# Kernel tuning notes

Hardware: AMD Instinct MI355X
Metric: run time of the kernel (lower is better)

The kernel has to match this reference:

```python
import jax, jax.numpy as jnp
import numpy as np

N_E = 8192
E_DIM = 256
BETA = 0.25
LAMBDA_REG = 0.1
UNIFORM_WEIGHT = 0.1


def setup_inputs() -> dict:
    key = jax.random.key(0)
    k1, k2 = jax.random.split(key)
    z = jax.random.normal(k1, (8, 2048, E_DIM), dtype=jnp.float32)
    # embedding initialized uniform(-1/n_e, 1/n_e) as in the torch module
    emb = jax.random.uniform(k2, (N_E, E_DIM), dtype=jnp.float32,
                             minval=-1.0 / N_E, maxval=1.0 / N_E)
    return {"z": z, "emb": emb}


def _safe_cdist(emb):
    # torch.cdist(emb, emb, p=2) with zero-safe sqrt (diag distances are 0)
    sq = jnp.sum(emb * emb, axis=1)  # [n_e]
    d2 = sq[:, None] + sq[None, :] - 2.0 * (emb @ emb.T)  # [n_e, n_e]
    d2 = jnp.maximum(d2, 0.0)
    pos = d2 > 0
    return jnp.where(pos, jnp.sqrt(jnp.where(pos, d2, 1.0)), 0.0)


def reference(z, emb):
    zf = z.reshape(-1, E_DIM)  # [N, e_dim]
    # squared-distance matrix: ||z||^2 + ||e||^2 - 2 z.e  -> [N, n_e]
    d = (jnp.sum(zf * zf, axis=1, keepdims=True)
         + jnp.sum(emb * emb, axis=1)
         - 2.0 * (zf @ emb.T))
    min_encoding_indices = jnp.argmin(d, axis=1)  # [N]
    # one-hot @ emb is just a gather of the selected codes
    z_q = emb[min_encoding_indices].reshape(z.shape)

    sg = jax.lax.stop_gradient
    loss = jnp.mean((sg(z_q) - z) ** 2) + BETA * jnp.mean((z_q - sg(z)) ** 2)
    z_q_st = z + sg(z_q - z)  # straight-through

    ed = _safe_cdist(emb)  # [n_e, n_e]
    min_d = jnp.min(ed, axis=1, keepdims=True)
    max_d = jnp.max(ed, axis=1, keepdims=True)
    uniform_loss = jnp.mean(max_d - min_d)
    qq_loss = UNIFORM_WEIGHT * uniform_loss + LAMBDA_REG * jnp.sum(emb * emb)

    return z_q_st, min_encoding_indices.reshape(-1, 1), loss, qq_loss
```

## Files before the change

### kernel.cpp

```cpp
#include <hip/hip_runtime.h>

#define D 256
#define DA 288
#define NKB 9
#define NKB_P 8
#define NE 8192
#define NZ 16384
#define BM 128
#define AM 256
#define BK 32
#define LDA (BM + 4)
#define NB (NE / BM)
#define NTRI (NB * (NB + 1) / 2)
#define NSPLIT_A 16
#define SPLIT_NA (NE / NSPLIT_A)
#define GAPTH_A 0.4096f
#define GAPTH_EFF 0.48f
#define LDM 17
#define NGB (NZ / 4)
#define NCH_A (SPLIT_NA / 32)
#define AUNITS (2 * NKB)
#define PUNITS (2 * NKB_P)
#define NBLK_ARG (NZ / AM * NSPLIT_A)
#define NBLK_BIG (NBLK_ARG + NTRI)

#define SROT(kk) (8 * ((((kk) >> 2)) & 3))
#define SWZR(kk, r) ((((r) + SROT(kk)) & 127))

typedef _Float16 f16x8 __attribute__((ext_vector_type(8)));
typedef _Float16 f16x4 __attribute__((ext_vector_type(4)));
typedef float f32x4 __attribute__((ext_vector_type(4)));

#define MFMA16(a, b, c) __builtin_amdgcn_mfma_f32_16x16x32_f16(a, b, c, 0, 0, 0)

__device__ __forceinline__ void g2l16(const void* g, void* lds) {
    __builtin_amdgcn_global_load_lds(
        (const __attribute__((address_space(1))) void*)g,
        (__attribute__((address_space(3))) void*)lds, 16, 0, 0);
}

__device__ __forceinline__ unsigned umax(unsigned a, unsigned b) { return a > b ? a : b; }
__device__ __forceinline__ unsigned umin(unsigned a, unsigned b) { return a < b ? a : b; }

#define WS_SUMS   0
#define WS_CNT    64
#define WS_ZSQ    256
#define WS_ESQ    (WS_ZSQ + NZ * 4)
#define WS_IDX    (WS_ESQ + NE * 4)
#define WS_KP1    (WS_IDX + NZ * 4)
#define WS_KP2    (WS_KP1 + NZ * NSPLIT_A * 4)
#define WS_RMX    (WS_KP2 + NZ * NSPLIT_A * 4)
#define WS_RMN    (WS_RMX + NE * 4)
#define WS_PACK   (WS_RMN + NE * 4)
#define WS_GPART  (WS_PACK + NZ * 8)
#define WS_LISTS  (WS_GPART + NGB * 8)
#define WS_ZHF    (WS_LISTS + NZ * NSPLIT_A * 4)
#define WS_EHF    (WS_ZHF + (size_t)(NZ / 16) * NKB * 64 * 8 * 2)
#define WS_CAND   WS_ZHF

__device__ __forceinline__ float waveReduceSumF(float v) {
    v += __shfl_down(v, 32); v += __shfl_down(v, 16); v += __shfl_down(v, 8);
    v += __shfl_down(v, 4);  v += __shfl_down(v, 2);  v += __shfl_down(v, 1);
    return v;
}
__device__ __forceinline__ double waveReduceSumD(double v) {
    v += __shfl_down(v, 32); v += __shfl_down(v, 16); v += __shfl_down(v, 8);
    v += __shfl_down(v, 4);  v += __shfl_down(v, 2);  v += __shfl_down(v, 1);
    return v;
}

__global__ __launch_bounds__(256) void k_setup(double* __restrict__ sums,
                                               int* __restrict__ cnt,
                                               unsigned* __restrict__ rmx,
                                               unsigned* __restrict__ rmn,
                                               unsigned long long* __restrict__ pack) {
    const int n = blockIdx.x * 256 + threadIdx.x;
    if (n == 0) {
        sums[0] = 0.0; sums[1] = 0.0; sums[2] = 0.0; sums[3] = 0.0;
#pragma unroll
        for (int s = 0; s < 24; ++s) cnt[s] = 0;
    }
    if (n < NE) { rmx[n] = 0u; rmn[n] = 0x7F800000u; }
    pack[n] = ~0ull;
}

__global__ __launch_bounds__(256) void k_rowsq(const float* __restrict__ src,
                                               float* __restrict__ rsq,
                                               double* __restrict__ sums) {
    const int row = blockIdx.x * 256 + threadIdx.x;
    const float* p = src + (size_t)row * D;
    float h[2];
#pragma unroll
    for (int half = 0; half < 2; ++half) {
        const float* q = p + half * 128;
        float4 a0 = *(const float4*)&q[0];
        float4 a1 = *(const float4*)&q[4];
        float r0 = __fmul_rn(a0.x, a0.x);
        float r1 = __fmul_rn(a0.y, a0.y);
        float r2 = __fmul_rn(a0.z, a0.z);
        float r3 = __fmul_rn(a0.w, a0.w);
        float r4 = __fmul_rn(a1.x, a1.x);
        float r5 = __fmul_rn(a1.y, a1.y);
        float r6 = __fmul_rn(a1.z, a1.z);
        float r7 = __fmul_rn(a1.w, a1.w);
#pragma unroll
        for (int i = 8; i < 128; i += 8) {
            const float4 b0 = *(const float4*)&q[i];
            const float4 b1 = *(const float4*)&q[i + 4];
            r0 = __fadd_rn(r0, __fmul_rn(b0.x, b0.x));
            r1 = __fadd_rn(r1, __fmul_rn(b0.y, b0.y));
            r2 = __fadd_rn(r2, __fmul_rn(b0.z, b0.z));
            r3 = __fadd_rn(r3, __fmul_rn(b0.w, b0.w));
            r4 = __fadd_rn(r4, __fmul_rn(b1.x, b1.x));
            r5 = __fadd_rn(r5, __fmul_rn(b1.y, b1.y));
            r6 = __fadd_rn(r6, __fmul_rn(b1.z, b1.z));
            r7 = __fadd_rn(r7, __fmul_rn(b1.w, b1.w));
        }
        const float t01 = __fadd_rn(r0, r1);
        const float t23 = __fadd_rn(r2, r3);
        const float t45 = __fadd_rn(r4, r5);
        const float t67 = __fadd_rn(r6, r7);
        h[half] = __fadd_rn(__fadd_rn(t01, t23), __fadd_rn(t45, t67));
    }
    const float tot = __fadd_rn(h[0], h[1]);
    rsq[row] = tot;
    if (sums != nullptr) {
        double s = waveReduceSumD((double)tot);
        if ((threadIdx.x & 63) == 0) atomicAdd(&sums[0], s);
    }
}

__global__ __launch_bounds__(256) void k_cvt_zf(const float* __restrict__ z,
                                                f16x8* __restrict__ zf) {
    __shared__ _Float16 Ls[64 * 296];
    const int t = threadIdx.x;
    const int row0 = blockIdx.x * 64;
#pragma unroll
    for (int i = 0; i < 16; ++i) {
        const int f4 = i * 256 + t;
        const int r = f4 >> 6, c4 = f4 & 63;
        const float4 v = *(const float4*)&z[(size_t)(row0 + r) * D + c4 * 4];
        f16x4 h;
        h[0] = (_Float16)v.x; h[1] = (_Float16)v.y;
        h[2] = (_Float16)v.z; h[3] = (_Float16)v.w;
        *(f16x4*)&Ls[r * 296 + c4 * 4] = h;
    }
#pragma unroll
    for (int i = 0; i < 8; ++i) {
        const int idx = i * 256 + t;
        const int r = idx >> 5, c = idx & 31;
        Ls[r * 296 + 256 + c] = (c <= 1) ? (_Float16)1.0f : (_Float16)0.0f;
    }
    __syncthreads();
    const int l = t & 63, w = t >> 6;
#pragma unroll
    for (int kb = 0; kb < NKB; ++kb) {
        const f16x8 fr = *(const f16x8*)&Ls[(w * 16 + (l & 15)) * 296 + kb * 32 + (l >> 4) * 8];
        zf[((size_t)(blockIdx.x * 4 + w) * NKB + kb) * 64 + l] = fr;
    }
}

__global__ __launch_bounds__(256) void k_cvt_ef(const float* __restrict__ e,
                                                const float* __restrict__ esq,
                                                f16x8* __restrict__ ef) {
    __shared__ _Float16 Ls[64 * 296];
    const int t = threadIdx.x;
    const int row0 = blockIdx.x * 64;
#pragma unroll
    for (int i = 0; i < 16; ++i) {
        const int f4 = i * 256 + t;
        const int r = f4 >> 6, c4 = f4 & 63;
        const float4 v = *(const float4*)&e[(size_t)(row0 + r) * D + c4 * 4];
        f16x4 h;
        h[0] = (_Float16)(v.x * 8192.0f); h[1] = (_Float16)(v.y * 8192.0f);
        h[2] = (_Float16)(v.z * 8192.0f); h[3] = (_Float16)(v.w * 8192.0f);
        *(f16x4*)&Ls[r * 296 + c4 * 4] = h;
    }
#pragma unroll
    for (int i = 0; i < 8; ++i) {
        const int idx = i * 256 + t;
        const int r = idx >> 5, c = idx & 31;
        _Float16 av = (_Float16)0.0f;
        if (c == 0) av = (_Float16)(esq[row0 + r] * -4096.0f);
        if (c == 1) av = (_Float16)512.0f;
        Ls[r * 296 + 256 + c] = av;
    }
    __syncthreads();
    const int l = t & 63, w = t >> 6;
#pragma unroll
    for (int kb = 0; kb < NKB; ++kb) {
        const f16x8 fr = *(const f16x8*)&Ls[(w * 16 + (l & 15)) * 296 + kb * 32 + (l >> 4) * 8];
        ef[((size_t)(blockIdx.x * 4 + w) * NKB + kb) * 64 + l] = fr;
    }
}

__global__ __launch_bounds__(256, 2) void k_big(
        const f16x8* __restrict__ zf, const f16x8* __restrict__ ef,
        const float* __restrict__ esq,
        unsigned* __restrict__ kp1, unsigned* __restrict__ kp2,
        unsigned* __restrict__ rmxg, unsigned* __restrict__ rmng) {
    __shared__ __align__(16) char Sh[2 * AUNITS * 1024];

    const int t = threadIdx.x;
    const int l = t & 63;
    const int w = t >> 6;
    const int quad = l >> 4;
    const int l15 = l & 15;

    if (blockIdx.x < NBLK_ARG) {
        _Float16 (*Bsm)[AUNITS * 512] = (_Float16(*)[AUNITS * 512])Sh;
        const int lin = blockIdx.x;
        const int rowblk = lin & 63;
        const int sp = lin >> 6;
        const int row0 = rowblk * AM;
        const int arb0 = rowblk * 16 + w * 4;

        f16x8 ah[4][NKB];
#pragma unroll
        for (int mi = 0; mi < 4; ++mi)
#pragma unroll
            for (int kb = 0; kb < NKB; ++kb)
                ah[mi][kb] = zf[((size_t)(arb0 + mi) * NKB + kb) * 64 + l];

        unsigned b1[16], b2[16];
#pragma unroll
        for (int s = 0; s < 16; ++s) { b1[s] = 0u; b2[s] = 0u; }

        const char* gp[5];
#pragma unroll
        for (int ui = 0; ui < 5; ++ui) {
            const int u = w + ui * 4;
            const int uc = (u < AUNITS) ? u : 0;
            const int nj = uc / NKB, kb = uc - nj * NKB;
            gp[ui] = (const char*)&ef[((size_t)(sp * 32 + nj) * NKB + kb) * 64 + l];
        }

        auto stage = [&](size_t choff, int buf) {
            char* lb = (char*)&Bsm[0][0] + buf * (AUNITS * 1024);
#pragma unroll
            for (int ui = 0; ui < 5; ++ui) {
                const int u = w + ui * 4;
                if (u < AUNITS) g2l16(gp[ui] + choff, lb + u * 1024);
            }
        };

        auto ins = [&](unsigned key, int s) {
            unsigned b2n;
            asm("v_med3_u32 %0, %1, %2, %3"
                : "=v"(b2n) : "v"(key), "v"(b1[s]), "v"(b2[s]));
            b2[s] = b2n;
            b1[s] = umax(b1[s], key);
        };

        stage(0, 0);
        const f32x4 Zv = (f32x4){0.f, 0.f, 0.f, 0.f};
        int inv0 = 1023 - l15;
        for (int ch = 0; ch < NCH_A; ++ch) {
            const int buf = ch & 1;
            __syncthreads();
            if (ch + 1 < NCH_A) stage((size_t)(ch + 1) * 18432u, buf ^ 1);

            const unsigned invA = (unsigned)inv0;
            const unsigned invB = (unsigned)(inv0 - 16);

            f32x4 acc0[4], acc1[4];
            {
                const f16x8 bh = *(const f16x8*)&Bsm[buf][(0 * NKB + 0) * 512 + l * 8];
#pragma unroll
                for (int mi = 0; mi < 4; ++mi) acc0[mi] = MFMA16(ah[mi][0], bh, Zv);
            }
#pragma unroll
            for (int kb = 1; kb < NKB; ++kb) {
                const f16x8 bh = *(const f16x8*)&Bsm[buf][(0 * NKB + kb) * 512 + l * 8];
#pragma unroll
                for (int mi = 0; mi < 4; ++mi) acc0[mi] = MFMA16(ah[mi][kb], bh, acc0[mi]);
            }
            {
                const f16x8 bh = *(const f16x8*)&Bsm[buf][(1 * NKB + 0) * 512 + l * 8];
#pragma unroll
                for (int mi = 0; mi < 4; ++mi) acc1[mi] = MFMA16(ah[mi][0], bh, Zv);
            }
#pragma unroll
            for (int kb = 1; kb < NKB; ++kb) {
                const f16x8 bh = *(const f16x8*)&Bsm[buf][(1 * NKB + kb) * 512 + l * 8];
#pragma unroll
                for (int mi = 0; mi < 4; ++mi) acc1[mi] = MFMA16(ah[mi][kb], bh, acc1[mi]);
#pragma unroll
                for (int e = 2 * (kb - 1); e < 2 * (kb - 1) + 2; ++e) {
                    const int mi0 = e >> 2, r0 = e & 3;
                    ins((__float_as_uint(acc0[mi0][r0]) & 0xFFFFFC00u) | invA, e);
                }
            }
#pragma unroll
            for (int mi = 0; mi < 4; ++mi)
#pragma unroll
                for (int r = 0; r < 4; ++r)
                    ins((__float_as_uint(acc1[mi][r]) & 0xFFFFFC00u) | invB, mi * 4 + r);

            inv0 -= 32;
        }

#pragma unroll
        for (int s = 0; s < 16; ++s) {
            unsigned v1 = b1[s], v2 = b2[s];
#pragma unroll
            for (int m = 1; m <= 8; m <<= 1) {
                const unsigned o1 = __shfl_xor(v1, m);
                const unsigned o2 = __shfl_xor(v2, m);
                const unsigned n2 = umax(umin(v1, o1), umax(v2, o2));
                v1 = umax(v1, o1);
                v2 = n2;
            }
            if (l15 == 0) {
                const int mi = s >> 2, r = s & 3;
                const int row = row0 + w * 64 + mi * 16 + quad * 4 + r;
                kp1[(size_t)row * NSPLIT_A + sp] = v1;
                kp2[(size_t)row * NSPLIT_A + sp] = v2;
            }
        }
    } else {
        _Float16 (*Bsm)[PUNITS * 512] = (_Float16(*)[PUNITS * 512])Sh;
        int p = blockIdx.x - NBLK_ARG;
        int bi = 0;
        while (p >= NB - bi) { p -= NB - bi; ++bi; }
        const int bj = bi + p;
        const int row0 = bi * BM;
        const int c0 = bj * BM;

        float sR[8], sC[8];
#pragma unroll
        for (int mi = 0; mi < 2; ++mi)
#pragma unroll
            for (int r = 0; r < 4; ++r)
                sR[mi * 4 + r] = esq[row0 + w * 32 + mi * 16 + quad * 4 + r];
#pragma unroll
        for (int nj = 0; nj < 8; ++nj) sC[nj] = esq[c0 + nj * 16 + l15];

        const int arb = bi * 8 + w * 2;
        const int cfb = bj * 8;

        f16x8 ah[2][NKB_P];
#pragma unroll
        for (int kb = 0; kb < NKB_P; ++kb) {
            ah[0][kb] = ef[((size_t)arb * NKB + kb) * 64 + l];
            ah[1][kb] = ef[((size_t)(arb + 1) * NKB + kb) * 64 + l];
        }

        float rmn[8], rmx[8], cmn[8], cmx[8];
#pragma unroll
        for (int s = 0; s < 8; ++s) { rmn[s] = 3.4e38f; rmx[s] = 0.f; cmn[s] = 3.4e38f; cmx[s] = 0.f; }

        auto stage = [&](int ch, int buf) {
            for (int u = w; u < PUNITS; u += 4) {
                const int nj = u >> 3, kb = u & 7;
                g2l16(&ef[((size_t)(cfb + ch * 2 + nj) * NKB + kb) * 64 + l],
                      &Bsm[buf][u * 512]);
            }
        };

        stage(0, 0);
        for (int ch = 0; ch < 4; ++ch) {
            const int buf = ch & 1;
            __syncthreads();
            if (ch + 1 < 4) stage(ch + 1, buf ^ 1);

            f32x4 acc[2][2];
#pragma unroll
            for (int mi = 0; mi < 2; ++mi)
#pragma unroll
                for (int nj = 0; nj < 2; ++nj) acc[mi][nj] = (f32x4){0.f, 0.f, 0.f, 0.f};

#pragma unroll
            for (int kb = 0; kb < NKB_P; ++kb) {
                const f16x8 bh0 = *(const f16x8*)&Bsm[buf][(0 * 8 + kb) * 512 + l * 8];
                const f16x8 bh1 = *(const f16x8*)&Bsm[buf][(1 * 8 + kb) * 512 + l * 8];
#pragma unroll
                for (int mi = 0; mi < 2; ++mi) {
                    acc[mi][0] = MFMA16(ah[mi][kb], bh0, acc[mi][0]);
                    acc[mi][1] = MFMA16(ah[mi][kb], bh1, acc[mi][1]);
                }
            }

#pragma unroll
            for (int nj = 0; nj < 2; ++nj) {
                const int cidx = ch * 2 + nj;
#pragma unroll
                for (int mi = 0; mi < 2; ++mi)
#pragma unroll
                    for (int r = 0; r < 4; ++r) {
                        const int s = mi * 4 + r;
                        const float t1 = __fadd_rn(sR[s], sC[cidx]);
                        const float d2 = fmaf(-0x1p-25f, acc[mi][nj][r], t1);
                        const float d2c = fmaxf(d2, 0.f);
                        rmn[s] = fminf(rmn[s], d2c);
                        rmx[s] = fmaxf(rmx[s], d2c);
                        cmn[cidx] = fminf(cmn[cidx], d2c);
                        cmx[cidx] = fmaxf(cmx[cidx], d2c);
                    }
            }
        }

#pragma unroll
        for (int s = 0; s < 8; ++s) {
#pragma unroll
            for (int m = 1; m <= 8; m <<= 1) {
                rmn[s] = fminf(rmn[s], __shfl_xor(rmn[s], m));
                rmx[s] = fmaxf(rmx[s], __shfl_xor(rmx[s], m));
            }
        }
        if (l15 == 0) {
#pragma unroll
            for (int s = 0; s < 8; ++s) {
                const int mi = s >> 2, r = s & 3;
                const int row = row0 + w * 32 + mi * 16 + quad * 4 + r;
                atomicMax(&rmxg[row], __float_as_uint(rmx[s]));
                atomicMin(&rmng[row], __float_as_uint(rmn[s]));
            }
        }

#pragma unroll
        for (int nj = 0; nj < 8; ++nj) {
#pragma unroll
            for (int m = 16; m <= 32; m <<= 1) {
                cmn[nj] = fminf(cmn[nj], __shfl_xor(cmn[nj], m));
                cmx[nj] = fmaxf(cmx[nj], __shfl_xor(cmx[nj], m));
            }
        }
        __syncthreads();
        float* Mn = (float*)&Bsm[0][0];
        float* Mx = (float*)&Bsm[0][0] + 512;
        if (quad == 0) {
#pragma unroll
            for (int nj = 0; nj < 8; ++nj) {
                Mn[w * 128 + nj * 16 + l15] = cmn[nj];
                Mx[w * 128 + nj * 16 + l15] = cmx[nj];
            }
        }
        __syncthreads();
        if (t < BM) {
            float mn = Mn[t], mx = Mx[t];
#pragma unroll
            for (int ww = 1; ww < 4; ++ww) {
                mn = fminf(mn, Mn[ww * 128 + t]);
                mx = fmaxf(mx, Mx[ww * 128 + t]);
            }
            atomicMax(&rmxg[c0 + t], __float_as_uint(mx));
            atomicMin(&rmng[c0 + t], __float_as_uint(mn));
        }
    }
}

__global__ __launch_bounds__(256) void k_merge(const unsigned* __restrict__ kp1,
                                               const unsigned* __restrict__ kp2,
                                               int* __restrict__ idxbuf,
                                               float* __restrict__ outidx,
                                               int* __restrict__ cnt,
                                               int* __restrict__ lists,
                                               unsigned long long* __restrict__ cand) {
    const int n = blockIdx.x * 256 + threadIdx.x;
    unsigned k1v[NSPLIT_A], k2v[NSPLIT_A];
#pragma unroll
    for (int s = 0; s < NSPLIT_A; ++s) {
        k1v[s] = kp1[n * NSPLIT_A + s];
        k2v[s] = kp2[n * NSPLIT_A + s];
    }
    unsigned K1 = k1v[0]; int sb = 0;
#pragma unroll
    for (int s = 1; s < NSPLIT_A; ++s)
        if (k1v[s] > K1) { K1 = k1v[s]; sb = s; }
    unsigned K2 = 0u;
#pragma unroll
    for (int s = 0; s < NSPLIT_A; ++s) {
        const unsigned a = (s == sb) ? k2v[s] : k1v[s];
        K2 = umax(K2, a);
    }
    const int ii1 = sb * SPLIT_NA + 1023 - (int)(K1 & 1023u);
    idxbuf[n] = ii1;
    outidx[n] = (float)ii1;
    const float val1 = __uint_as_float(K1 & 0xFFFFFC00u);
    const float val2 = __uint_as_float(K2 & 0xFFFFFC00u);
    if (val1 - val2 < GAPTH_EFF) {
        const float vlim = val1 - GAPTH_EFF;
        int ncand = 0;
#pragma unroll
        for (int s = 0; s < NSPLIT_A; ++s) {
            if (__uint_as_float(k1v[s] & 0xFFFFFC00u) >= vlim) ++ncand;
            if (__uint_as_float(k2v[s] & 0xFFFFFC00u) >= vlim) {
                const int p = atomicAdd(&cnt[s], 1);
                lists[s * NZ + p] = n;
            }
        }
        const int base = atomicAdd(&cnt[16], ncand);
        int o = 0;
#pragma unroll
        for (int s = 0; s < NSPLIT_A; ++s)
            if (__uint_as_float(k1v[s] & 0xFFFFFC00u) >= vlim) {
                const int col = s * SPLIT_NA + 1023 - (int)(k1v[s] & 1023u);
                cand[base + o] = ((unsigned long long)(unsigned)n << 32) |
                                 (unsigned)col;
                ++o;
            }
    }
}

__global__ __launch_bounds__(256) void k_fix_cand(const float* __restrict__ z,
                                                  const float* __restrict__ emb,
                                                  const float* __restrict__ zsq,
                                                  const float* __restrict__ esq,
                                                  const int* __restrict__ cnt,
                                                  const unsigned long long* __restrict__ cand,
                                                  unsigned long long* __restrict__ pack) {
    const int nc = cnt[16];
    for (int i = blockIdx.x * 256 + threadIdx.x; i < nc; i += gridDim.x * 256) {
        const unsigned long long pr = cand[i];
        const int row = (int)(pr >> 32);
        const int col = (int)(pr & 0xffffffffu);
        const float4* zp = (const float4*)(z + (size_t)row * D);
        const float4* ep = (const float4*)(emb + (size_t)col * D);
        float acc = 0.f;
#pragma unroll
        for (int k4 = 0; k4 < D / 4; ++k4) {
            const float4 a = zp[k4];
            const float4 b = ep[k4];
            acc = fmaf(a.x, b.x, acc);
            acc = fmaf(a.y, b.y, acc);
            acc = fmaf(a.z, b.z, acc);
            acc = fmaf(a.w, b.w, acc);
        }
        const float sc = fmaf(-2.f, acc, __fadd_rn(zsq[row], esq[col]));
        const unsigned long long pk =
            ((unsigned long long)__float_as_uint(sc) << 32) | (unsigned)col;
        atomicMin(&pack[row], pk);
    }
}

__global__ __launch_bounds__(256) void k_fix_split(const float* __restrict__ z,
                                                   const float* __restrict__ emb,
                                                   const float* __restrict__ zsq,
                                                   const float* __restrict__ esq,
                                                   const int* __restrict__ cnt,
                                                   const int* __restrict__ lists,
                                                   unsigned long long* __restrict__ pack) {
    __shared__ float As[BK * LDA];
    __shared__ float Bs[BK * LDA];
    __shared__ float Sq[BM];
    __shared__ int frow[BM];

    const int s = blockIdx.x >> 2;
    const int chunk = blockIdx.x & 3;
    const int ns = cnt[s];
    const int c0 = s * SPLIT_NA + chunk * BM;
    const int t = threadIdx.x;
    const int tr = t >> 4;
    const int tc = t & 15;
    const int sr = t >> 3;
    const int skq = t & 7;
    const int wrot = 8 * (skq & 3);

    for (int rb = blockIdx.y; rb * BM < ns; rb += gridDim.y) {
        __syncthreads();
        if (t < BM) {
            const int fi = rb * BM + t;
            frow[t] = (fi < ns) ? lists[s * NZ + fi] : lists[s * NZ];
            Sq[t] = esq[c0 + t];
        }
        __syncthreads();

        float zqr[8];
#pragma unroll
        for (int i = 0; i < 8; ++i) zqr[i] = zsq[frow[tr * 8 + i]];

        float best[8];
        int bidx[8];
#pragma unroll
        for (int i = 0; i < 8; ++i) { best[i] = 3.4e38f; bidx[i] = 0; }

        float acc[8][8];
#pragma unroll
        for (int i = 0; i < 8; ++i)
#pragma unroll
            for (int j = 0; j < 8; ++j) acc[i][j] = 0.f;

        float4 pav[4], pbv[4];
#pragma unroll
        for (int q = 0; q < 4; ++q) {
            const int r = sr + 32 * q;
            pav[q] = *(const float4*)&z[(size_t)frow[r] * D + 0 + 4 * skq];
            pbv[q] = *(const float4*)&emb[(size_t)(c0 + r) * D + 0 + 4 * skq];
        }

        for (int kb = 0; kb < D; kb += BK) {
            __syncthreads();
#pragma unroll
            for (int q = 0; q < 4; ++q) {
                const int r = sr + 32 * q;
                const int rr = (r + wrot) & 127;
                As[(4 * skq + 0) * LDA + rr] = pav[q].x;
                As[(4 * skq + 1) * LDA + rr] = pav[q].y;
                As[(4 * skq + 2) * LDA + rr] = pav[q].z;
                As[(4 * skq + 3) * LDA + rr] = pav[q].w;
                Bs[(4 * skq + 0) * LDA + rr] = pbv[q].x;
                Bs[(4 * skq + 1) * LDA + rr] = pbv[q].y;
                Bs[(4 * skq + 2) * LDA + rr] = pbv[q].z;
                Bs[(4 * skq + 3) * LDA + rr] = pbv[q].w;
            }
            __syncthreads();
            if (kb + BK < D) {
#pragma unroll
                for (int q = 0; q < 4; ++q) {
                    const int r = sr + 32 * q;
                    pav[q] = *(const float4*)&z[(size_t)frow[r] * D + kb + BK + 4 * skq];
                    pbv[q] = *(const float4*)&emb[(size_t)(c0 + r) * D + kb + BK + 4 * skq];
                }
            }
#pragma unroll
            for (int k = 0; k < BK; ++k) {
                const float4 a0 = *(const float4*)&As[k * LDA + SWZR(k, tr * 8)];
                const float4 a1 = *(const float4*)&As[k * LDA + SWZR(k, tr * 8 + 4)];
                const float4 b0 = *(const float4*)&Bs[k * LDA + SWZR(k, tc * 4)];
                const float4 b1 = *(const float4*)&Bs[k * LDA + SWZR(k, 64 + tc * 4)];
                const float a[8] = {a0.x, a0.y, a0.z, a0.w, a1.x, a1.y, a1.z, a1.w};
                const float b[8] = {b0.x, b0.y, b0.z, b0.w, b1.x, b1.y, b1.z, b1.w};
#pragma unroll
                for (int i = 0; i < 8; ++i)
#pragma unroll
                    for (int j = 0; j < 8; ++j)
                        acc[i][j] = fmaf(a[i], b[j], acc[i][j]);
            }
        }
#pragma unroll
        for (int jj = 0; jj < 8; ++jj) {
            const int cloc = (jj < 4) ? (tc * 4 + jj) : (64 + tc * 4 + (jj - 4));
            const float sq = Sq[cloc];
            const int gcol = c0 + cloc;
#pragma unroll
            for (int i = 0; i < 8; ++i) {
                const float t1 = __fadd_rn(zqr[i], sq);
                const float sc = fmaf(-2.f, acc[i][jj], t1);
                if (sc < best[i]) { best[i] = sc; bidx[i] = gcol; }
            }
        }
        __syncthreads();

        float* Rs = As;
        int* Ri = (int*)Bs;
#pragma unroll
        for (int i = 0; i < 8; ++i) {
            Rs[(tr * 8 + i) * LDM + tc] = best[i];
            Ri[(tr * 8 + i) * LDM + tc] = bidx[i];
        }
        __syncthreads();
        if (t < BM) {
            float bs = Rs[t * LDM];
            int bi = Ri[t * LDM];
#pragma unroll
            for (int c = 1; c < 16; ++c) {
                const float sc = Rs[t * LDM + c];
                const int ii = Ri[t * LDM + c];
                if (sc < bs || (sc == bs && ii < bi)) { bs = sc; bi = ii; }
            }
            const int fi = rb * BM + t;
            if (fi < ns) {
                const unsigned long long pk =
                    ((unsigned long long)__float_as_uint(bs) << 32) | (unsigned)bi;
                atomicMin(&pack[frow[t]], pk);
            }
        }
    }
}

__global__ __launch_bounds__(256) void k_gather(const float* __restrict__ z,
                                                const float* __restrict__ emb,
                                                const int* __restrict__ idxbuf,
                                                const unsigned long long* __restrict__ pack,
                                                float* __restrict__ out,
                                                float* __restrict__ outidx,
                                                double* __restrict__ gpart) {
    __shared__ double part[4];
    const int row = blockIdx.x * 4 + (threadIdx.x >> 6);
    const int lane = threadIdx.x & 63;
    const unsigned long long p = pack[row];
    const int idx = (p != ~0ull) ? (int)(p & 0xffffffffu) : idxbuf[row];
    if (lane == 0) outidx[row] = (float)idx;
    const float4 e4 = *(const float4*)&emb[(size_t)idx * D + lane * 4];
    const float4 z4 = *(const float4*)&z[(size_t)row * D + lane * 4];
    *(float4*)&out[(size_t)row * D + lane * 4] = e4;
    const float dx = e4.x - z4.x, dy = e4.y - z4.y;
    const float dzv = e4.z - z4.z, dw = e4.w - z4.w;
    float s = dx * dx + dy * dy + dzv * dzv + dw * dw;
    s = waveReduceSumF(s);
    if (lane == 0) part[threadIdx.x >> 6] = (double)s;
    __syncthreads();
    if (threadIdx.x == 0)
        gpart[blockIdx.x] = part[0] + part[1] + part[2] + part[3];
}

__global__ __launch_bounds__(256) void k_final(const double* __restrict__ sums,
                                               const double* __restrict__ gpart,
                                               const unsigned* __restrict__ rmxg,
                                               const unsigned* __restrict__ rmng,
                                               float* __restrict__ out) {
    __shared__ double part[4];
    __shared__ double partm[4];
    const int t = threadIdx.x;
    double s = 0.0;
#pragma unroll
    for (int i = 0; i < NGB / 256; ++i) s += gpart[i * 256 + t];
    s = waveReduceSumD(s);
    double m = 0.0;
#pragma unroll
    for (int i = 0; i < NE / 256; ++i) {
        const int n = i * 256 + t;
        const float mx = sqrtf(__uint_as_float(rmxg[n]));
        const float mn = sqrtf(__uint_as_float(rmng[n]));
        m += (double)(mx - mn);
    }
    m = waveReduceSumD(m);
    if ((t & 63) == 0) { part[t >> 6] = s; partm[t >> 6] = m; }
    __syncthreads();
    if (t == 0) {
        const double diff2 = part[0] + part[1] + part[2] + part[3];
        const double msum = partm[0] + partm[1] + partm[2] + partm[3];
        const double loss = 1.25 * (diff2 / (double)((size_t)NZ * D));
        const double qq = 0.1 * (msum / (double)NE) + 0.1 * sums[0];
        out[(size_t)NZ * D + NZ] = (float)loss;
        out[(size_t)NZ * D + NZ + 1] = (float)qq;
    }
}

extern "C" void kernel_launch(void* const* d_in, const int* in_sizes, int n_in,
                              void* d_out, int out_size, void* d_ws, size_t ws_size,
                              hipStream_t stream) {
    const float* z = (const float*)d_in[0];
    const float* emb = (const float*)d_in[1];
    float* out = (float*)d_out;
    char* ws = (char*)d_ws;

    double* sums = (double*)(ws + WS_SUMS);
    int* cnt = (int*)(ws + WS_CNT);
    float* zsq = (float*)(ws + WS_ZSQ);
    float* esq = (float*)(ws + WS_ESQ);
    int* idxb = (int*)(ws + WS_IDX);
    unsigned* kp1 = (unsigned*)(ws + WS_KP1);
    unsigned* kp2 = (unsigned*)(ws + WS_KP2);
    unsigned* rmx = (unsigned*)(ws + WS_RMX);
    unsigned* rmn = (unsigned*)(ws + WS_RMN);
    unsigned long long* pack = (unsigned long long*)(ws + WS_PACK);
    double* gpart = (double*)(ws + WS_GPART);
    int* lists = (int*)(ws + WS_LISTS);
    f16x8* zhf = (f16x8*)(ws + WS_ZHF);
    f16x8* ehf = (f16x8*)(ws + WS_EHF);
    unsigned long long* cand = (unsigned long long*)(ws + WS_CAND);
    float* outidx = out + (size_t)NZ * D;

    hipLaunchKernelGGL(k_setup, dim3(NZ / 256), dim3(256), 0, stream,
                       sums, cnt, rmx, rmn, pack);
    hipLaunchKernelGGL(k_rowsq, dim3(NZ / 256), dim3(256), 0, stream, z, zsq, (double*)nullptr);
    hipLaunchKernelGGL(k_rowsq, dim3(NE / 256), dim3(256), 0, stream, emb, esq, sums);
    hipLaunchKernelGGL(k_cvt_zf, dim3(NZ / 64), dim3(256), 0, stream, z, zhf);
    hipLaunchKernelGGL(k_cvt_ef, dim3(NE / 64), dim3(256), 0, stream, emb, esq, ehf);
    hipLaunchKernelGGL(k_big, dim3(NBLK_BIG), dim3(256), 0, stream,
                       zhf, ehf, esq, kp1, kp2, rmx, rmn);
    hipLaunchKernelGGL(k_merge, dim3(NZ / 256), dim3(256), 0, stream,
                       kp1, kp2, idxb, outidx, cnt, lists, cand);
    hipLaunchKernelGGL(k_fix_cand, dim3(128), dim3(256), 0, stream,
                       z, emb, zsq, esq, cnt, cand, pack);
    hipLaunchKernelGGL(k_fix_split, dim3(64, 16), dim3(256), 0, stream,
                       z, emb, zsq, esq, cnt, lists, pack);
    hipLaunchKernelGGL(k_gather, dim3(NGB), dim3(256), 0, stream,
                       z, emb, idxb, pack, out, outidx, gpart);
    hipLaunchKernelGGL(k_final, dim3(1), dim3(256), 0, stream,
                       sums, gpart, rmx, rmn, out);
}
```

Baseline: 286.3 us.

## Drop row-min tracking in pairwise distance, fuse prep kernels

Removes the per-row minimum of the codebook self-distance matrix, relying on the diagonal being zero, so the min reductions and atomicMin calls in the triangle blocks disappear. Merges the setup, row-norm and fp16 conversion kernels into two launches. The codebook squared-norm sum moves into the final kernel instead of using atomics. The risk is a small numeric difference if the reference's diagonal distance is not exactly zero.

After: 253.8 us. 11.4% less time.

```diff
diff --git a/kernel.cpp b/kernel.cpp
--- a/kernel.cpp
+++ b/kernel.cpp
@@ -69,26 +69,7 @@
     return v;
 }
 
-__global__ __launch_bounds__(256) void k_setup(double* __restrict__ sums,
-                                               int* __restrict__ cnt,
-                                               unsigned* __restrict__ rmx,
-                                               unsigned* __restrict__ rmn,
-                                               unsigned long long* __restrict__ pack) {
-    const int n = blockIdx.x * 256 + threadIdx.x;
-    if (n == 0) {
-        sums[0] = 0.0; sums[1] = 0.0; sums[2] = 0.0; sums[3] = 0.0;
-#pragma unroll
-        for (int s = 0; s < 24; ++s) cnt[s] = 0;
-    }
-    if (n < NE) { rmx[n] = 0u; rmn[n] = 0x7F800000u; }
-    pack[n] = ~0ull;
-}
-
-__global__ __launch_bounds__(256) void k_rowsq(const float* __restrict__ src,
-                                               float* __restrict__ rsq,
-                                               double* __restrict__ sums) {
-    const int row = blockIdx.x * 256 + threadIdx.x;
-    const float* p = src + (size_t)row * D;
+__device__ __forceinline__ float rowsq256(const float* __restrict__ p) {
     float h[2];
 #pragma unroll
     for (int half = 0; half < 2; ++half) {
@@ -122,75 +103,91 @@
         const float t67 = __fadd_rn(r6, r7);
         h[half] = __fadd_rn(__fadd_rn(t01, t23), __fadd_rn(t45, t67));
     }
-    const float tot = __fadd_rn(h[0], h[1]);
-    rsq[row] = tot;
-    if (sums != nullptr) {
-        double s = waveReduceSumD((double)tot);
-        if ((threadIdx.x & 63) == 0) atomicAdd(&sums[0], s);
-    }
-}
-
-__global__ __launch_bounds__(256) void k_cvt_zf(const float* __restrict__ z,
-                                                f16x8* __restrict__ zf) {
+    return __fadd_rn(h[0], h[1]);
+}
+
+__global__ __launch_bounds__(256) void k_pre(const float* __restrict__ z,
+                                             const float* __restrict__ emb,
+                                             float* __restrict__ zsq,
+                                             float* __restrict__ esq,
+                                             int* __restrict__ cnt,
+                                             unsigned* __restrict__ rmx,
+                                             unsigned long long* __restrict__ pack) {
+    const int bx = blockIdx.x, t = threadIdx.x;
+    if (bx == 0 && t < 24) cnt[t] = 0;
+    if (bx < 64) {
+        const int row = bx * 256 + t;
+        zsq[row] = rowsq256(z + (size_t)row * D);
+        pack[row] = ~0ull;
+    } else {
+        const int row = (bx - 64) * 256 + t;
+        esq[row] = rowsq256(emb + (size_t)row * D);
+        rmx[row] = 0u;
+    }
+}
+
+__global__ __launch_bounds__(256) void k_cvt(const float* __restrict__ z,
+                                             const float* __restrict__ e,
+                                             const float* __restrict__ esq,
+                                             f16x8* __restrict__ zf,
+                                             f16x8* __restrict__ ef) {
     __shared__ _Float16 Ls[64 * 296];
     const int t = threadIdx.x;
-    const int row0 = blockIdx.x * 64;
-#pragma unroll
-    for (int i = 0; i < 16; ++i) {
-        const int f4 = i * 256 + t;
-        const int r = f4 >> 6, c4 = f4 & 63;
-        const float4 v = *(const float4*)&z[(size_t)(row0 + r) * D + c4 * 4];
-        f16x4 h;
-        h[0] = (_Float16)v.x; h[1] = (_Float16)v.y;
-        h[2] = (_Float16)v.z; h[3] = (_Float16)v.w;
-        *(f16x4*)&Ls[r * 296 + c4 * 4] = h;
-    }
-#pragma unroll
-    for (int i = 0; i < 8; ++i) {
-        const int idx = i * 256 + t;
-        const int r = idx >> 5, c = idx & 31;
-        Ls[r * 296 + 256 + c] = (c <= 1) ? (_Float16)1.0f : (_Float16)0.0f;
-    }
-    __syncthreads();
-    const int l = t & 63, w = t >> 6;
-#pragma unroll
-    for (int kb = 0; kb < NKB; ++kb) {
-        const f16x8 fr = *(const f16x8*)&Ls[(w * 16 + (l & 15)) * 296 + kb * 32 + (l >> 4) * 8];
-        zf[((size_t)(blockIdx.x * 4 + w) * NKB + kb) * 64 + l] = fr;
-    }
-}
-
-__global__ __launch_bounds__(256) void k_cvt_ef(const float* __restrict__ e,
-                                                const float* __restrict__ esq,
-                                                f16x8* __restrict__ ef) {
-    __shared__ _Float16 Ls[64 * 296];
-    const int t = threadIdx.x;
-    const int row0 = blockIdx.x * 64;
-#pragma unroll
-    for (int i = 0; i < 16; ++i) {
-        const int f4 = i * 256 + t;
-        const int r = f4 >> 6, c4 = f4 & 63;
-        const float4 v = *(const float4*)&e[(size_t)(row0 + r) * D + c4 * 4];
-        f16x4 h;
-        h[0] = (_Float16)(v.x * 8192.0f); h[1] = (_Float16)(v.y * 8192.0f);
-        h[2] = (_Float16)(v.z * 8192.0f); h[3] = (_Float16)(v.w * 8192.0f);
-        *(f16x4*)&Ls[r * 296 + c4 * 4] = h;
-    }
-#pragma unroll
-    for (int i = 0; i < 8; ++i) {
-        const int idx = i * 256 + t;
-        const int r = idx >> 5, c = idx & 31;
-        _Float16 av = (_Float16)0.0f;
-        if (c == 0) av = (_Float16)(esq[row0 + r] * -4096.0f);
-        if (c == 1) av = (_Float16)512.0f;
-        Ls[r * 296 + 256 + c] = av;
-    }
-    __syncthreads();
-    const int l = t & 63, w = t >> 6;
-#pragma unroll
-    for (int kb = 0; kb < NKB; ++kb) {
-        const f16x8 fr = *(const f16x8*)&Ls[(w * 16 + (l & 15)) * 296 + kb * 32 + (l >> 4) * 8];
-        ef[((size_t)(blockIdx.x * 4 + w) * NKB + kb) * 64 + l] = fr;
+    const int bx = blockIdx.x;
+    if (bx < NZ / 64) {
+        const int row0 = bx * 64;
+#pragma unroll
+        for (int i = 0; i < 16; ++i) {
+            const int f4 = i * 256 + t;
+            const int r = f4 >> 6, c4 = f4 & 63;
+            const float4 v = *(const float4*)&z[(size_t)(row0 + r) * D + c4 * 4];
+            f16x4 h;
+            h[0] = (_Float16)v.x; h[1] = (_Float16)v.y;
+            h[2] = (_Float16)v.z; h[3] = (_Float16)v.w;
+            *(f16x4*)&Ls[r * 296 + c4 * 4] = h;
+        }
+#pragma unroll
+        for (int i = 0; i < 8; ++i) {
+            const int idx = i * 256 + t;
+            const int r = idx >> 5, c = idx & 31;
+            Ls[r * 296 + 256 + c] = (c <= 1) ? (_Float16)1.0f : (_Float16)0.0f;
+        }
+        __syncthreads();
+        const int l = t & 63, w = t >> 6;
+#pragma unroll
+        for (int kb = 0; kb < NKB; ++kb) {
+            const f16x8 fr = *(const f16x8*)&Ls[(w * 16 + (l & 15)) * 296 + kb * 32 + (l >> 4) * 8];
+            zf[((size_t)(bx * 4 + w) * NKB + kb) * 64 + l] = fr;
+        }
+    } else {
+        const int eb = bx - NZ / 64;
+        const int row0 = eb * 64;
+#pragma unroll
+        for (int i = 0; i < 16; ++i) {
+            const int f4 = i * 256 + t;
+            const int r = f4 >> 6, c4 = f4 & 63;
+            const float4 v = *(const float4*)&e[(size_t)(row0 + r) * D + c4 * 4];
+            f16x4 h;
+            h[0] = (_Float16)(v.x * 8192.0f); h[1] = (_Float16)(v.y * 8192.0f);
+            h[2] = (_Float16)(v.z * 8192.0f); h[3] = (_Float16)(v.w * 8192.0f);
+            *(f16x4*)&Ls[r * 296 + c4 * 4] = h;
+        }
+#pragma unroll
+        for (int i = 0; i < 8; ++i) {
+            const int idx = i * 256 + t;
+            const int r = idx >> 5, c = idx & 31;
+            _Float16 av = (_Float16)0.0f;
+            if (c == 0) av = (_Float16)(esq[row0 + r] * -4096.0f);
+            if (c == 1) av = (_Float16)512.0f;
+            Ls[r * 296 + 256 + c] = av;
+        }
+        __syncthreads();
+        const int l = t & 63, w = t >> 6;
+#pragma unroll
+        for (int kb = 0; kb < NKB; ++kb) {
+            const f16x8 fr = *(const f16x8*)&Ls[(w * 16 + (l & 15)) * 296 + kb * 32 + (l >> 4) * 8];
+            ef[((size_t)(eb * 4 + w) * NKB + kb) * 64 + l] = fr;
+        }
     }
 }
 
@@ -198,7 +195,7 @@
         const f16x8* __restrict__ zf, const f16x8* __restrict__ ef,
         const float* __restrict__ esq,
         unsigned* __restrict__ kp1, unsigned* __restrict__ kp2,
-        unsigned* __restrict__ rmxg, unsigned* __restrict__ rmng) {
+        unsigned* __restrict__ rmxg) {
     __shared__ __align__(16) char Sh[2 * AUNITS * 1024];
 
     const int t = threadIdx.x;
@@ -346,9 +343,9 @@
             ah[1][kb] = ef[((size_t)(arb + 1) * NKB + kb) * 64 + l];
         }
 
-        float rmn[8], rmx[8], cmn[8], cmx[8];
-#pragma unroll
-        for (int s = 0; s < 8; ++s) { rmn[s] = 3.4e38f; rmx[s] = 0.f; cmn[s] = 3.4e38f; cmx[s] = 0.f; }
+        float rmx[8], cmx[8];
+#pragma unroll
+        for (int s = 0; s < 8; ++s) { rmx[s] = 0.f; cmx[s] = 0.f; }
 
         auto stage = [&](int ch, int buf) {
             for (int u = w; u < PUNITS; u += 4) {
@@ -392,9 +389,7 @@
                         const float t1 = __fadd_rn(sR[s], sC[cidx]);
                         const float d2 = fmaf(-0x1p-25f, acc[mi][nj][r], t1);
                         const float d2c = fmaxf(d2, 0.f);
-                        rmn[s] = fminf(rmn[s], d2c);
                         rmx[s] = fmaxf(rmx[s], d2c);
-                        cmn[cidx] = fminf(cmn[cidx], d2c);
                         cmx[cidx] = fmaxf(cmx[cidx], d2c);
                     }
             }
@@ -403,10 +398,8 @@
 #pragma unroll
         for (int s = 0; s < 8; ++s) {
 #pragma unroll
-            for (int m = 1; m <= 8; m <<= 1) {
-                rmn[s] = fminf(rmn[s], __shfl_xor(rmn[s], m));
+            for (int m = 1; m <= 8; m <<= 1)
                 rmx[s] = fmaxf(rmx[s], __shfl_xor(rmx[s], m));
-            }
         }
         if (l15 == 0) {
 #pragma unroll
@@ -414,38 +407,29 @@
                 const int mi = s >> 2, r = s & 3;
                 const int row = row0 + w * 32 + mi * 16 + quad * 4 + r;
                 atomicMax(&rmxg[row], __float_as_uint(rmx[s]));
-                atomicMin(&rmng[row], __float_as_uint(rmn[s]));
             }
         }
 
 #pragma unroll
         for (int nj = 0; nj < 8; ++nj) {
 #pragma unroll
-            for (int m = 16; m <= 32; m <<= 1) {
-                cmn[nj] = fminf(cmn[nj], __shfl_xor(cmn[nj], m));
+            for (int m = 16; m <= 32; m <<= 1)
                 cmx[nj] = fmaxf(cmx[nj], __shfl_xor(cmx[nj], m));
-            }
         }
         __syncthreads();
-        float* Mn = (float*)&Bsm[0][0];
-        float* Mx = (float*)&Bsm[0][0] + 512;
+        float* Mx = (float*)&Bsm[0][0];
         if (quad == 0) {
 #pragma unroll
-            for (int nj = 0; nj < 8; ++nj) {
-                Mn[w * 128 + nj * 16 + l15] = cmn[nj];
+            for (int nj = 0; nj < 8; ++nj)
                 Mx[w * 128 + nj * 16 + l15] = cmx[nj];
-            }
         }
         __syncthreads();
         if (t < BM) {
-            float mn = Mn[t], mx = Mx[t];
-#pragma unroll
-            for (int ww = 1; ww < 4; ++ww) {
-                mn = fminf(mn, Mn[ww * 128 + t]);
+            float mx = Mx[t];
+#pragma unroll
+            for (int ww = 1; ww < 4; ++ww)
                 mx = fmaxf(mx, Mx[ww * 128 + t]);
-            }
             atomicMax(&rmxg[c0 + t], __float_as_uint(mx));
-            atomicMin(&rmng[c0 + t], __float_as_uint(mn));
         }
     }
 }
@@ -695,34 +679,35 @@
         gpart[blockIdx.x] = part[0] + part[1] + part[2] + part[3];
 }
 
-__global__ __launch_bounds__(256) void k_final(const double* __restrict__ sums,
-                                               const double* __restrict__ gpart,
+__global__ __launch_bounds__(256) void k_final(const double* __restrict__ gpart,
+                                               const float* __restrict__ esq,
                                                const unsigned* __restrict__ rmxg,
-                                               const unsigned* __restrict__ rmng,
                                                float* __restrict__ out) {
     __shared__ double part[4];
     __shared__ double partm[4];
+    __shared__ double parte[4];
     const int t = threadIdx.x;
     double s = 0.0;
 #pragma unroll
     for (int i = 0; i < NGB / 256; ++i) s += gpart[i * 256 + t];
     s = waveReduceSumD(s);
-    double m = 0.0;
+    double m = 0.0, e2 = 0.0;
 #pragma unroll
     for (int i = 0; i < NE / 256; ++i) {
         const int n = i * 256 + t;
-        const float mx = sqrtf(__uint_as_float(rmxg[n]));
-        const float mn = sqrtf(__uint_as_float(rmng[n]));
-        m += (double)(mx - mn);
+        m += (double)sqrtf(__uint_as_float(rmxg[n]));
+        e2 += (double)esq[n];
     }
     m = waveReduceSumD(m);
-    if ((t & 63) == 0) { part[t >> 6] = s; partm[t >> 6] = m; }
+    e2 = waveReduceSumD(e2);
+    if ((t & 63) == 0) { part[t >> 6] = s; partm[t >> 6] = m; parte[t >> 6] = e2; }
     __syncthreads();
     if (t == 0) {
         const double diff2 = part[0] + part[1] + part[2] + part[3];
         const double msum = partm[0] + partm[1] + partm[2] + partm[3];
+        const double esum = parte[0] + parte[1] + parte[2] + parte[3];
         const double loss = 1.25 * (diff2 / (double)((size_t)NZ * D));
-        const double qq = 0.1 * (msum / (double)NE) + 0.1 * sums[0];
+        const double qq = 0.1 * (msum / (double)NE) + 0.1 * esum;
         out[(size_t)NZ * D + NZ] = (float)loss;
         out[(size_t)NZ * D + NZ + 1] = (float)qq;
     }
@@ -736,7 +721,6 @@
     float* out = (float*)d_out;
     char* ws = (char*)d_ws;
 
-    double* sums = (double*)(ws + WS_SUMS);
     int* cnt = (int*)(ws + WS_CNT);
     float* zsq = (float*)(ws + WS_ZSQ);
     float* esq = (float*)(ws + WS_ESQ);
@@ -744,7 +728,6 @@
     unsigned* kp1 = (unsigned*)(ws + WS_KP1);
     unsigned* kp2 = (unsigned*)(ws + WS_KP2);
     unsigned* rmx = (unsigned*)(ws + WS_RMX);
-    unsigned* rmn = (unsigned*)(ws + WS_RMN);
     unsigned long long* pack = (unsigned long long*)(ws + WS_PACK);
     double* gpart = (double*)(ws + WS_GPART);
     int* lists = (int*)(ws + WS_LISTS);
@@ -753,14 +736,12 @@
     unsigned long long* cand = (unsigned long long*)(ws + WS_CAND);
     float* outidx = out + (size_t)NZ * D;
 
-    hipLaunchKernelGGL(k_setup, dim3(NZ / 256), dim3(256), 0, stream,
-                       sums, cnt, rmx, rmn, pack);
-    hipLaunchKernelGGL(k_rowsq, dim3(NZ / 256), dim3(256), 0, stream, z, zsq, (double*)nullptr);
-    hipLaunchKernelGGL(k_rowsq, dim3(NE / 256), dim3(256), 0, stream, emb, esq, sums);
-    hipLaunchKernelGGL(k_cvt_zf, dim3(NZ / 64), dim3(256), 0, stream, z, zhf);
-    hipLaunchKernelGGL(k_cvt_ef, dim3(NE / 64), dim3(256), 0, stream, emb, esq, ehf);
+    hipLaunchKernelGGL(k_pre, dim3(96), dim3(256), 0, stream,
+                       z, emb, zsq, esq, cnt, rmx, pack);
+    hipLaunchKernelGGL(k_cvt, dim3(NZ / 64 + NE / 64), dim3(256), 0, stream,
+                       z, emb, esq, zhf, ehf);
     hipLaunchKernelGGL(k_big, dim3(NBLK_BIG), dim3(256), 0, stream,
-                       zhf, ehf, esq, kp1, kp2, rmx, rmn);
+                       zhf, ehf, esq, kp1, kp2, rmx);
     hipLaunchKernelGGL(k_merge, dim3(NZ / 256), dim3(256), 0, stream,
                        kp1, kp2, idxb, outidx, cnt, lists, cand);
     hipLaunchKernelGGL(k_fix_cand, dim3(128), dim3(256), 0, stream,
@@ -770,5 +751,5 @@
     hipLaunchKernelGGL(k_gather, dim3(NGB), dim3(256), 0, stream,
                        z, emb, idxb, pack, out, outidx, gpart);
     hipLaunchKernelGGL(k_final, dim3(1), dim3(256), 0, stream,
-                       sums, gpart, rmx, rmn, out);
-}
+                       gpart, esq, rmx, out);
+}
```
